# Performance work log

Hardware: AMD Instinct MI355X
Metric: run time of the kernel (lower is better)

Reference implementation:

```python
import jax, jax.numpy as jnp
import numpy as np

LOG_SQRT_2PI = 0.9189385332046727  # log(sqrt(2*pi))
PI_MIX = 0.5
SIGMA1 = 1.0
SIGMA2 = 0.002

B, IN, OUT = 64, 1024, 1024


def setup_inputs() -> dict:
    key = jax.random.key(0)
    ks = jax.random.split(key, 7)
    x = jax.random.normal(ks[0], (B, IN), jnp.float32)
    weight_mu = jax.random.uniform(ks[1], (OUT, IN), jnp.float32, -0.2, 0.2)
    weight_rho = jax.random.uniform(ks[2], (OUT, IN), jnp.float32, -5.0, -4.0)
    bias_mu = jax.random.uniform(ks[3], (OUT,), jnp.float32, -0.2, 0.2)
    bias_rho = jax.random.uniform(ks[4], (OUT,), jnp.float32, -5.0, -4.0)
    eps_w = jax.random.normal(ks[5], (B, OUT, IN), jnp.float32)  # per-row weight noise
    eps_b = jax.random.normal(ks[6], (B, OUT), jnp.float32)      # per-row bias noise
    return {"x": x, "weight_mu": weight_mu, "weight_rho": weight_rho,
            "bias_mu": bias_mu, "bias_rho": bias_rho, "eps_w": eps_w, "eps_b": eps_b}


def _posterior_log_prob(value, mu, sigma):
    # GaussianParameters.log_prob, summed over all elements (incl. batch)
    return jnp.sum(-LOG_SQRT_2PI - jnp.log(sigma) - (value - mu) ** 2 / (2.0 * sigma ** 2))


def _mixture_log_prob(value):
    # zero-mean two-component scale-mixture prior: pi*N(0,s1) + (1-pi)*N(0,s2)
    lp1 = -LOG_SQRT_2PI - jnp.log(jnp.float32(SIGMA1)) - value ** 2 / jnp.float32(2.0 * SIGMA1 ** 2)
    lp2 = -LOG_SQRT_2PI - jnp.log(jnp.float32(SIGMA2)) - value ** 2 / jnp.float32(2.0 * SIGMA2 ** 2)
    return jnp.sum(jnp.logaddexp(jnp.log(jnp.float32(PI_MIX)) + lp1,
                                 jnp.log(jnp.float32(1.0 - PI_MIX)) + lp2))


def reference(x, weight_mu, weight_rho, bias_mu, bias_rho, eps_w, eps_b):
    # sigma = log1p(exp(rho))  (softplus reparameterization)
    w_sigma = jax.nn.softplus(weight_rho)            # (O, I)
    b_sigma = jax.nn.softplus(bias_rho)              # (O,)
    # per-sample weight/bias draws ('sample' branch, vectorized over batch)
    weight = weight_mu[None] + w_sigma[None] * eps_w  # (B, O, I)
    bias = bias_mu[None] + b_sigma[None] * eps_b      # (B, O)
    out = jnp.einsum('boi,bi->bo', weight, x) + bias  # (B, O)
    log_prior = _mixture_log_prob(weight) + _mixture_log_prob(bias)
    log_posterior = (_posterior_log_prob(weight, weight_mu[None], w_sigma[None])
                     + _posterior_log_prob(bias, bias_mu[None], b_sigma[None]))
    return out, log_prior, log_posterior
```

## Files before the change

### kernel.cpp

```cpp
#include <hip/hip_runtime.h>

#define B_    64
#define IN_   1024
#define OUT_  1024
#define NROWS (B_ * OUT_)

#define LOG2E_F 1.4426950408889634f
#define LN2_F   0.6931471805599453f
#define LN2_D   0.6931471805599453
#define LSQ2PI_D 0.9189385332046727
#define CA2_D  (-2.3257480647361595)
#define CA2_F  (-2.3257481f)
#define A1_2_D (-0.7213475204444817)
#define A1_2_F (-0.72134752f)
#define NDS2_F (-180336.159f)
#define NDC2_F (8.965784284662087f)

#define N_ACC 384

__device__ __forceinline__ float fexp2(float x) {
#if __has_builtin(__builtin_amdgcn_exp2f)
    return __builtin_amdgcn_exp2f(x);
#else
    return exp2f(x);
#endif
}
__device__ __forceinline__ float flog2(float x) {
#if __has_builtin(__builtin_amdgcn_logf)
    return __builtin_amdgcn_logf(x);
#else
    return __log2f(x);
#endif
}
__device__ __forceinline__ float softterm(float t) {
    return flog2(1.0f + fexp2(t));
}
__device__ __forceinline__ float softplusf(float r) {
    return LN2_F * softterm(r * LOG2E_F);
}

__device__ __forceinline__ float wred(float v) {
#pragma unroll
    for (int o = 32; o > 0; o >>= 1) v += __shfl_down(v, o, 64);
    return v;
}

__global__ __launch_bounds__(384) void k_zero(double* __restrict__ acc) {
    int t = threadIdx.x;
    if (t < N_ACC) acc[t] = 0.0;
}

#define COMP(EC, XC, SGC, MUC)                                                \
    {                                                                         \
        float w  = fmaf(SGC, EC, MUC);                                        \
        dot      = fmaf(w, XC, dot);                                          \
        float v2 = w * w;                                                     \
        sw2 += v2;                                                            \
        soft += softterm(fmaf(NDS2_F, v2, NDC2_F));                           \
        ep2 = fmaf(EC, EC, ep2);                                              \
    }

__global__ __launch_bounds__(256) void k_main(const float* __restrict__ x,
                                              const float* __restrict__ wmu,
                                              const float* __restrict__ wrho,
                                              const float* __restrict__ bmu,
                                              const float* __restrict__ brho,
                                              const float* __restrict__ epsw,
                                              const float* __restrict__ epsb,
                                              float* __restrict__ out,
                                              double* __restrict__ acc) {
    const int lane = threadIdx.x & 63;
    const int wid  = threadIdx.x >> 6;
    const int gw   = blockIdx.x * 4 + wid;
    const int o    = gw & 1023;
    const int b0   = gw >> 10;

    const float4* mp = (const float4*)(wmu  + (size_t)o * IN_);
    const float4* rp = (const float4*)(wrho + (size_t)o * IN_);

    float4 sg[4], mu[4];
#pragma unroll
    for (int k = 0; k < 4; ++k) {
        float4 r = rp[lane + 64 * k];
        mu[k]    = mp[lane + 64 * k];
        sg[k].x  = softplusf(r.x);
        sg[k].y  = softplusf(r.y);
        sg[k].z  = softplusf(r.z);
        sg[k].w  = softplusf(r.w);
    }

    float lsg = 0.f;
    if (b0 == 0) {
#pragma unroll
        for (int k = 0; k < 4; ++k)
            lsg += flog2(sg[k].x) + flog2(sg[k].y) + flog2(sg[k].z) + flog2(sg[k].w);
    }

    float sgb = 0.f, l2sgb = 0.f, bm = 0.f;
    if (lane == 0) {
        float rb = brho[o];
        sgb   = softplusf(rb);
        l2sgb = flog2(sgb);
        bm    = bmu[o];
    }

    float soft = 0.f, sw2 = 0.f, ep2 = 0.f, pb2 = 0.f, postb = 0.f;
#pragma unroll
    for (int j = 0; j < 4; ++j) {
        const int b      = b0 + 16 * j;
        const size_t row = ((size_t)b << 10) | (size_t)o;
        const float4* ep = (const float4*)(epsw + row * IN_);
        const float4* xp = (const float4*)(x + ((size_t)b << 10));
        float dot = 0.f;
#pragma unroll
        for (int k = 0; k < 4; ++k) {
            float4 e  = ep[lane + 64 * k];
            float4 xx = xp[lane + 64 * k];
            COMP(e.x, xx.x, sg[k].x, mu[k].x)
            COMP(e.y, xx.y, sg[k].y, mu[k].y)
            COMP(e.z, xx.z, sg[k].z, mu[k].z)
            COMP(e.w, xx.w, sg[k].w, mu[k].w)
        }
        dot = wred(dot);
        if (lane == 0) {
            float eb = epsb[row];
            float bv = fmaf(sgb, eb, bm);
            out[row] = dot + bv;
            float v2b = bv * bv;
            pb2  += fmaf(A1_2_F, v2b, CA2_F) + softterm(fmaf(NDS2_F, v2b, NDC2_F));
            postb += fmaf(-LN2_F, l2sgb, -0.5f * eb * eb);
        }
    }

    soft = wred(soft);
    ep2  = wred(ep2);
    sw2  = wred(sw2);
    if (b0 == 0) lsg = wred(lsg);

    __shared__ float sm[6][4];
    if (lane == 0) {
        sm[0][wid] = soft;
        sm[1][wid] = ep2;
        sm[2][wid] = sw2;
        sm[3][wid] = pb2;
        sm[4][wid] = postb;
        sm[5][wid] = lsg;
    }
    __syncthreads();
    if (threadIdx.x < 6) {
        int s   = threadIdx.x;
        float v = sm[s][0] + sm[s][1] + sm[s][2] + sm[s][3];
        if (s < 5 || blockIdx.x < 256)
            atomicAdd(&acc[s * 64 + (blockIdx.x & 63)], (double)v);
    }
}

__global__ void k_fin(const double* __restrict__ acc, float* __restrict__ out) {
    int t = threadIdx.x;
    double v[6];
#pragma unroll
    for (int s = 0; s < 6; ++s) v[s] = acc[s * 64 + t];
#pragma unroll
    for (int o = 32; o > 0; o >>= 1) {
#pragma unroll
        for (int s = 0; s < 6; ++s) v[s] += __shfl_down(v[s], o, 64);
    }
    if (t == 0) {
        double soft2 = v[0], eps2 = v[1], sw2 = v[2];
        double p2b = v[3], postb = v[4], lsig2 = v[5];
        double NW = 67108864.0;
        double log_prior = LN2_D * (soft2 + A1_2_D * sw2 + NW * CA2_D + p2b);
        double log_post  = -NW * LSQ2PI_D - 64.0 * (LN2_D * lsig2) - 0.5 * eps2
                           + postb - 65536.0 * LSQ2PI_D;
        out[NROWS]     = (float)log_prior;
        out[NROWS + 1] = (float)log_post;
    }
}

extern "C" void kernel_launch(void* const* d_in, const int* in_sizes, int n_in,
                              void* d_out, int out_size, void* d_ws, size_t ws_size,
                              hipStream_t stream) {
    const float* x    = (const float*)d_in[0];
    const float* wmu  = (const float*)d_in[1];
    const float* wrho = (const float*)d_in[2];
    const float* bmu  = (const float*)d_in[3];
    const float* brho = (const float*)d_in[4];
    const float* epsw = (const float*)d_in[5];
    const float* epsb = (const float*)d_in[6];
    float* out  = (float*)d_out;
    double* acc = (double*)d_ws;

    k_zero<<<1, 384, 0, stream>>>(acc);
    k_main<<<NROWS / 16, 256, 0, stream>>>(x, wmu, wrho, bmu, brho, epsw, epsb, out, acc);
    k_fin<<<1, 64, 0, stream>>>(acc, out);
}
```

Baseline: 400.6 us.

## Use nontemporal eps loads, per-block partials, fused shuffle reductions, drop zero kernel

```diff
diff --git a/kernel.cpp b/kernel.cpp
--- a/kernel.cpp
+++ b/kernel.cpp
@@ -3,7 +3,8 @@
 #define B_    64
 #define IN_   1024
 #define OUT_  1024
-#define NROWS (B_ * OUT_)
+#define NROWS 65536
+#define NBLK  4096
 
 #define LOG2E_F 1.4426950408889634f
 #define LN2_F   0.6931471805599453f
@@ -16,21 +17,16 @@
 #define NDS2_F (-180336.159f)
 #define NDC2_F (8.965784284662087f)
 
-#define N_ACC 384
-
+typedef float f32x4 __attribute__((ext_vector_type(4)));
+
+__device__ __forceinline__ f32x4 ntld(const f32x4* p) {
+    return __builtin_nontemporal_load(p);
+}
 __device__ __forceinline__ float fexp2(float x) {
-#if __has_builtin(__builtin_amdgcn_exp2f)
     return __builtin_amdgcn_exp2f(x);
-#else
-    return exp2f(x);
-#endif
 }
 __device__ __forceinline__ float flog2(float x) {
-#if __has_builtin(__builtin_amdgcn_logf)
     return __builtin_amdgcn_logf(x);
-#else
-    return __log2f(x);
-#endif
 }
 __device__ __forceinline__ float softterm(float t) {
     return flog2(1.0f + fexp2(t));
@@ -39,25 +35,30 @@
     return LN2_F * softterm(r * LOG2E_F);
 }
 
-__device__ __forceinline__ float wred(float v) {
-#pragma unroll
-    for (int o = 32; o > 0; o >>= 1) v += __shfl_down(v, o, 64);
-    return v;
-}
-
-__global__ __launch_bounds__(384) void k_zero(double* __restrict__ acc) {
-    int t = threadIdx.x;
-    if (t < N_ACC) acc[t] = 0.0;
-}
-
-#define COMP(EC, XC, SGC, MUC)                                                \
+#define COMP(EC, XC, SGC, MUC, DOT)                                           \
     {                                                                         \
         float w  = fmaf(SGC, EC, MUC);                                        \
-        dot      = fmaf(w, XC, dot);                                          \
+        DOT      = fmaf(w, XC, DOT);                                          \
         float v2 = w * w;                                                     \
         sw2 += v2;                                                            \
         soft += softterm(fmaf(NDS2_F, v2, NDC2_F));                           \
         ep2 = fmaf(EC, EC, ep2);                                              \
+    }
+
+#define ROWJ(JB, DOT)                                                         \
+    {                                                                         \
+        const size_t bb_ = (size_t)(b0 + (JB));                               \
+        const f32x4* ep  = (const f32x4*)(epsw + (((bb_ << 10) | (size_t)o) << 10)); \
+        const f32x4* xp  = (const f32x4*)(x + (bb_ << 10));                   \
+        _Pragma("unroll")                                                     \
+        for (int k = 0; k < 4; ++k) {                                         \
+            f32x4 e  = ntld(ep + lane + 64 * k);                              \
+            f32x4 xx = xp[lane + 64 * k];                                     \
+            COMP(e.x, xx.x, sg[k].x, mu[k].x, DOT)                            \
+            COMP(e.y, xx.y, sg[k].y, mu[k].y, DOT)                            \
+            COMP(e.z, xx.z, sg[k].z, mu[k].z, DOT)                            \
+            COMP(e.w, xx.w, sg[k].w, mu[k].w, DOT)                            \
+        }                                                                     \
     }
 
 __global__ __launch_bounds__(256) void k_main(const float* __restrict__ x,
@@ -68,25 +69,25 @@
                                               const float* __restrict__ epsw,
                                               const float* __restrict__ epsb,
                                               float* __restrict__ out,
-                                              double* __restrict__ acc) {
+                                              float* __restrict__ ws) {
     const int lane = threadIdx.x & 63;
     const int wid  = threadIdx.x >> 6;
     const int gw   = blockIdx.x * 4 + wid;
     const int o    = gw & 1023;
     const int b0   = gw >> 10;
 
-    const float4* mp = (const float4*)(wmu  + (size_t)o * IN_);
-    const float4* rp = (const float4*)(wrho + (size_t)o * IN_);
-
-    float4 sg[4], mu[4];
+    const f32x4* mp = (const f32x4*)(wmu  + (size_t)o * IN_);
+    const f32x4* rp = (const f32x4*)(wrho + (size_t)o * IN_);
+
+    f32x4 sg[4], mu[4];
 #pragma unroll
     for (int k = 0; k < 4; ++k) {
-        float4 r = rp[lane + 64 * k];
-        mu[k]    = mp[lane + 64 * k];
-        sg[k].x  = softplusf(r.x);
-        sg[k].y  = softplusf(r.y);
-        sg[k].z  = softplusf(r.z);
-        sg[k].w  = softplusf(r.w);
+        f32x4 r = rp[lane + 64 * k];
+        mu[k]   = mp[lane + 64 * k];
+        sg[k].x = softplusf(r.x);
+        sg[k].y = softplusf(r.y);
+        sg[k].z = softplusf(r.z);
+        sg[k].w = softplusf(r.w);
     }
 
     float lsg = 0.f;
@@ -96,46 +97,46 @@
             lsg += flog2(sg[k].x) + flog2(sg[k].y) + flog2(sg[k].z) + flog2(sg[k].w);
     }
 
-    float sgb = 0.f, l2sgb = 0.f, bm = 0.f;
-    if (lane == 0) {
-        float rb = brho[o];
-        sgb   = softplusf(rb);
-        l2sgb = flog2(sgb);
-        bm    = bmu[o];
-    }
-
-    float soft = 0.f, sw2 = 0.f, ep2 = 0.f, pb2 = 0.f, postb = 0.f;
-#pragma unroll
-    for (int j = 0; j < 4; ++j) {
-        const int b      = b0 + 16 * j;
-        const size_t row = ((size_t)b << 10) | (size_t)o;
-        const float4* ep = (const float4*)(epsw + row * IN_);
-        const float4* xp = (const float4*)(x + ((size_t)b << 10));
-        float dot = 0.f;
-#pragma unroll
-        for (int k = 0; k < 4; ++k) {
-            float4 e  = ep[lane + 64 * k];
-            float4 xx = xp[lane + 64 * k];
-            COMP(e.x, xx.x, sg[k].x, mu[k].x)
-            COMP(e.y, xx.y, sg[k].y, mu[k].y)
-            COMP(e.z, xx.z, sg[k].z, mu[k].z)
-            COMP(e.w, xx.w, sg[k].w, mu[k].w)
-        }
-        dot = wred(dot);
-        if (lane == 0) {
-            float eb = epsb[row];
-            float bv = fmaf(sgb, eb, bm);
-            out[row] = dot + bv;
-            float v2b = bv * bv;
-            pb2  += fmaf(A1_2_F, v2b, CA2_F) + softterm(fmaf(NDS2_F, v2b, NDC2_F));
-            postb += fmaf(-LN2_F, l2sgb, -0.5f * eb * eb);
-        }
-    }
-
-    soft = wred(soft);
-    ep2  = wred(ep2);
-    sw2  = wred(sw2);
-    if (b0 == 0) lsg = wred(lsg);
+    float sgb   = softplusf(brho[o]);
+    float l2sgb = flog2(sgb);
+    float bm    = bmu[o];
+
+    float dot0 = 0.f, dot1 = 0.f, dot2 = 0.f, dot3 = 0.f;
+    float soft = 0.f, sw2 = 0.f, ep2 = 0.f;
+
+    ROWJ(0,  dot0)
+    ROWJ(16, dot1)
+    ROWJ(32, dot2)
+    ROWJ(48, dot3)
+
+    float bv = 0.f, pb2 = 0.f, postb = 0.f;
+    const int bb = b0 + 16 * lane;
+    if (lane < 4) {
+        float eb  = epsb[((size_t)bb << 10) | (size_t)o];
+        bv        = fmaf(sgb, eb, bm);
+        float v2b = bv * bv;
+        pb2   = fmaf(A1_2_F, v2b, CA2_F) + softterm(fmaf(NDS2_F, v2b, NDC2_F));
+        postb = fmaf(-LN2_F, l2sgb, -0.5f * eb * eb);
+    }
+
+#pragma unroll
+    for (int off = 32; off; off >>= 1) {
+        dot0 += __shfl_xor(dot0, off, 64);
+        dot1 += __shfl_xor(dot1, off, 64);
+        dot2 += __shfl_xor(dot2, off, 64);
+        dot3 += __shfl_xor(dot3, off, 64);
+        soft += __shfl_xor(soft, off, 64);
+        sw2  += __shfl_xor(sw2,  off, 64);
+        ep2  += __shfl_xor(ep2,  off, 64);
+        lsg  += __shfl_xor(lsg,  off, 64);
+        pb2  += __shfl_xor(pb2,  off, 64);
+        postb+= __shfl_xor(postb,off, 64);
+    }
+
+    if (lane < 4) {
+        float d = (lane == 0) ? dot0 : (lane == 1) ? dot1 : (lane == 2) ? dot2 : dot3;
+        out[((size_t)bb << 10) | (size_t)o] = d + bv;
+    }
 
     __shared__ float sm[6][4];
     if (lane == 0) {
@@ -148,27 +149,41 @@
     }
     __syncthreads();
     if (threadIdx.x < 6) {
-        int s   = threadIdx.x;
-        float v = sm[s][0] + sm[s][1] + sm[s][2] + sm[s][3];
-        if (s < 5 || blockIdx.x < 256)
-            atomicAdd(&acc[s * 64 + (blockIdx.x & 63)], (double)v);
-    }
-}
-
-__global__ void k_fin(const double* __restrict__ acc, float* __restrict__ out) {
-    int t = threadIdx.x;
-    double v[6];
-#pragma unroll
-    for (int s = 0; s < 6; ++s) v[s] = acc[s * 64 + t];
-#pragma unroll
-    for (int o = 32; o > 0; o >>= 1) {
-#pragma unroll
-        for (int s = 0; s < 6; ++s) v[s] += __shfl_down(v[s], o, 64);
-    }
+        int s = threadIdx.x;
+        ws[s * NBLK + blockIdx.x] = sm[s][0] + sm[s][1] + sm[s][2] + sm[s][3];
+    }
+}
+
+__global__ __launch_bounds__(256) void k_fin(const float* __restrict__ ws,
+                                             float* __restrict__ out) {
+    const int t    = threadIdx.x;
+    const int lane = t & 63;
+    const int wid  = t >> 6;
+    double a[6] = {0, 0, 0, 0, 0, 0};
+    for (int i = 0; i < 16; ++i) {
+        int idx = t + 256 * i;
+#pragma unroll
+        for (int s = 0; s < 6; ++s) a[s] += (double)ws[s * NBLK + idx];
+    }
+#pragma unroll
+    for (int off = 32; off; off >>= 1) {
+#pragma unroll
+        for (int s = 0; s < 6; ++s) a[s] += __shfl_xor(a[s], off, 64);
+    }
+    __shared__ double sm[6][4];
+    if (lane == 0) {
+#pragma unroll
+        for (int s = 0; s < 6; ++s) sm[s][wid] = a[s];
+    }
+    __syncthreads();
     if (t == 0) {
+        double v[6];
+#pragma unroll
+        for (int s = 0; s < 6; ++s)
+            v[s] = sm[s][0] + sm[s][1] + sm[s][2] + sm[s][3];
         double soft2 = v[0], eps2 = v[1], sw2 = v[2];
         double p2b = v[3], postb = v[4], lsig2 = v[5];
-        double NW = 67108864.0;
+        const double NW = 67108864.0;
         double log_prior = LN2_D * (soft2 + A1_2_D * sw2 + NW * CA2_D + p2b);
         double log_post  = -NW * LSQ2PI_D - 64.0 * (LN2_D * lsig2) - 0.5 * eps2
                            + postb - 65536.0 * LSQ2PI_D;
@@ -187,10 +202,9 @@
     const float* brho = (const float*)d_in[4];
     const float* epsw = (const float*)d_in[5];
     const float* epsb = (const float*)d_in[6];
-    float* out  = (float*)d_out;
-    double* acc = (double*)d_ws;
-
-    k_zero<<<1, 384, 0, stream>>>(acc);
-    k_main<<<NROWS / 16, 256, 0, stream>>>(x, wmu, wrho, bmu, brho, epsw, epsb, out, acc);
-    k_fin<<<1, 64, 0, stream>>>(acc, out);
-}
+    float* out = (float*)d_out;
+    float* ws  = (float*)d_ws;
+
+    k_main<<<NBLK, 256, 0, stream>>>(x, wmu, wrho, bmu, brho, epsw, epsb, out, ws);
+    k_fin<<<1, 256, 0, stream>>>(ws, out);
+}
```

New measurement: 373.0 us. -6.9%, faster.
